# Kernel optimization log

Hardware: AMD Instinct MI355X
Metric: run time of the kernel (lower is better)

Reference implementation:

```python
import jax, jax.numpy as jnp
import numpy as np

B, H, K, NUM_PTR, MAX_LEN = 32768, 896, 2000, 2, 128


def setup_inputs() -> dict:
    key = jax.random.key(0)
    k1, k2, k3 = jax.random.split(key, 3)
    z = jax.random.normal(k1, (B, H), dtype=jnp.float32)
    # codebook init: normal(0, 0.02) as in torch.nn.init.normal_
    emb = 0.02 * jax.random.normal(k2, (K, H), dtype=jnp.float32)
    # pointer heads: two Linear(H, MAX_LEN) layers, stacked
    W = jax.random.normal(k3, (NUM_PTR, MAX_LEN, H), dtype=jnp.float32) / np.float32(np.sqrt(H))
    b = jnp.zeros((NUM_PTR, MAX_LEN), dtype=jnp.float32)
    return {"z": z, "emb": emb, "W": W, "b": b, "prompt_len": 96}


def reference(z, emb, W, b, prompt_len):
    # --- quantize: L2 cdist + argmin + gather + straight-through ---
    # dist[b,k] = ||z_b||^2 - 2 z_b . e_k + ||e_k||^2   -> [B, K]
    dist = (jnp.sum(z * z, axis=1, keepdims=True)
            - 2.0 * (z @ emb.T)
            + jnp.sum(emb * emb, axis=1)[None, :])
    idx = jnp.argmin(dist, axis=1)            # [B]
    z_q = emb[idx]                            # [B, H]
    op_state = z + jax.lax.stop_gradient(z_q - z)
    # --- pointer heads with prompt-length mask ---
    logits = jnp.einsum('bh,plh->bpl', z, W) + b[None, :, :]   # [B, 2, MAX_LEN]
    mask = jnp.where(jnp.arange(logits.shape[-1]) < prompt_len, 0.0, -jnp.inf)
    ptr_logits = logits + mask[None, None, :]
    return op_state, ptr_logits
```

## Files before the change

### kernel.cpp

```cpp
#include <hip/hip_runtime.h>
#include <hip/hip_bf16.h>
#include <cstdint>
#include <cstddef>

#define B_SZ 32768
#define H_SZ 896
#define K_SZ 2000
#define KPAD 2048
#define NPTR_COLS 256
#define NCAT 2304
#define BM 128
#define BN 128
#define BK 32
#define TPS 6

typedef float floatx4 __attribute__((ext_vector_type(4)));
typedef __bf16 bf16x8 __attribute__((ext_vector_type(8)));

#define MASK_NEG 1.0e30f

__device__ inline unsigned short f2bf_rne(float x) {
  unsigned u = __builtin_bit_cast(unsigned, x);
  unsigned r = u + 0x7fffu + ((u >> 16) & 1u);
  return (unsigned short)(r >> 16);
}
__device__ inline float bf2f(unsigned short b) {
  unsigned u = ((unsigned)b) << 16;
  return __builtin_bit_cast(float, u);
}

typedef __attribute__((address_space(1))) void GV;
typedef __attribute__((address_space(3))) void LV;
__device__ inline void load_lds16(const void* gsrc, void* ldst) {
  __builtin_amdgcn_global_load_lds((GV*)gsrc, (LV*)ldst, 16, 0, 0);
}

__global__ __launch_bounds__(256) void convert_kernel(
    const float* __restrict__ emb, const float* __restrict__ W,
    unsigned short* __restrict__ cat_hi, unsigned short* __restrict__ cat_lo,
    float* __restrict__ normE) {
  const int row = blockIdx.x;
  const int tid = threadIdx.x;
  const float* src = nullptr;
  bool zero = false;
  if (row < K_SZ)       src = emb + (size_t)row * H_SZ;
  else if (row < KPAD)  zero = true;
  else                  src = W + (size_t)(row - KPAD) * H_SZ;

  float ss = 0.f;
  for (int c = tid; c < H_SZ; c += 256) {
    float x = zero ? 0.f : src[c];
    unsigned short hb = f2bf_rne(x);
    float hf = bf2f(hb);
    unsigned short lb = f2bf_rne(x - hf);
    cat_hi[(size_t)row * H_SZ + c] = hb;
    cat_lo[(size_t)row * H_SZ + c] = lb;
    ss += x * x;
  }
  #pragma unroll
  for (int off = 32; off > 0; off >>= 1) ss += __shfl_down(ss, off);
  __shared__ float wsum[4];
  const int wave = tid >> 6, lane = tid & 63;
  if (lane == 0) wsum[wave] = ss;
  __syncthreads();
  if (tid == 0 && row < KPAD) normE[row] = wsum[0] + wsum[1] + wsum[2] + wsum[3];
}

__global__ __launch_bounds__(256) void convert_z(
    const float* __restrict__ z,
    unsigned short* __restrict__ zhi, unsigned short* __restrict__ zlo) {
  const size_t t = (size_t)blockIdx.x * 256 + threadIdx.x;
  const float* src = z + t * 8;
  float x[8];
  *(float4*)&x[0] = *(const float4*)src;
  *(float4*)&x[4] = *(const float4*)(src + 4);
  unsigned hv[4], lv[4];
  #pragma unroll
  for (int q = 0; q < 4; ++q) {
    unsigned short h0 = f2bf_rne(x[2 * q]), h1 = f2bf_rne(x[2 * q + 1]);
    float r0 = x[2 * q] - bf2f(h0), r1 = x[2 * q + 1] - bf2f(h1);
    unsigned short l0 = f2bf_rne(r0), l1 = f2bf_rne(r1);
    hv[q] = (unsigned)h0 | ((unsigned)h1 << 16);
    lv[q] = (unsigned)l0 | ((unsigned)l1 << 16);
  }
  *(uint4*)(zhi + t * 8) = make_uint4(hv[0], hv[1], hv[2], hv[3]);
  *(uint4*)(zlo + t * 8) = make_uint4(lv[0], lv[1], lv[2], lv[3]);
}

__global__ __launch_bounds__(256, 2) void main_gemm(
    const unsigned short* __restrict__ zhi,
    const unsigned short* __restrict__ zlo,
    const unsigned short* __restrict__ cat_hi,
    const unsigned short* __restrict__ cat_lo,
    const float* __restrict__ normE,
    const float* __restrict__ bias,
    const int* __restrict__ plen_p,
    float* __restrict__ pmin, int* __restrict__ pidx,
    float* __restrict__ out_logits) {
  __shared__ unsigned short Ahi[BM * BK], Alo[BM * BK];
  __shared__ unsigned short Bhi[BN * BK], Blo[BN * BK];
  __shared__ float red_v[2][BM];
  __shared__ int   red_i[2][BM];

  const int tid = threadIdx.x;
  const int wave = tid >> 6, lane = tid & 63;
  const int wm = wave >> 1, wn = wave & 1;
  const int bx = blockIdx.x, split = blockIdx.y;
  const int b0 = bx * BM;
  const int lrow = lane & 15, lk = lane >> 4;
  const int csw = ((lk ^ ((lrow >> 1) & 3)) << 3);

  const int srow = lane >> 2;
  const int scol = (((lane & 3) ^ ((lane >> 3) & 3)) << 3);

  float minv[16];
  int   mini[16];
  #pragma unroll
  for (int s = 0; s < 16; ++s) { minv[s] = 3.4e38f; mini[s] = 0; }

  const unsigned short* pa_hi[2];
  const unsigned short* pa_lo[2];
  #pragma unroll
  for (int s = 0; s < 2; ++s) {
    const int seg = wave * 2 + s;
    const size_t off = (size_t)(b0 + seg * 16 + srow) * H_SZ + scol;
    pa_hi[s] = zhi + off;
    pa_lo[s] = zlo + off;
  }

  const int t0 = split * TPS;
  for (int tt = t0; tt < t0 + TPS; ++tt) {
    const int n0 = tt * BN;
    const unsigned short* pb_hi[2];
    const unsigned short* pb_lo[2];
    #pragma unroll
    for (int s = 0; s < 2; ++s) {
      const int seg = wave * 2 + s;
      const size_t off = (size_t)(n0 + seg * 16 + srow) * H_SZ + scol;
      pb_hi[s] = cat_hi + off;
      pb_lo[s] = cat_lo + off;
    }

    floatx4 acc[4][4];
    #pragma unroll
    for (int i = 0; i < 4; ++i)
      #pragma unroll
      for (int j = 0; j < 4; ++j) acc[i][j] = (floatx4){0.f, 0.f, 0.f, 0.f};

    for (int kk = 0; kk < H_SZ; kk += BK) {
      #pragma unroll
      for (int s = 0; s < 2; ++s) {
        const int seg = wave * 2 + s;
        load_lds16(pa_hi[s] + kk, &Ahi[seg * 512]);
        load_lds16(pa_lo[s] + kk, &Alo[seg * 512]);
        load_lds16(pb_hi[s] + kk, &Bhi[seg * 512]);
        load_lds16(pb_lo[s] + kk, &Blo[seg * 512]);
      }
      __syncthreads();

      bf16x8 ah[4], al[4], bh[4], bl[4];
      #pragma unroll
      for (int i = 0; i < 4; ++i) {
        const int r = (wm * 64 + i * 16 + lrow) * BK + csw;
        ah[i] = *(const bf16x8*)&Ahi[r];
        al[i] = *(const bf16x8*)&Alo[r];
      }
      #pragma unroll
      for (int j = 0; j < 4; ++j) {
        const int r = (wn * 64 + j * 16 + lrow) * BK + csw;
        bh[j] = *(const bf16x8*)&Bhi[r];
        bl[j] = *(const bf16x8*)&Blo[r];
      }
      #pragma unroll
      for (int i = 0; i < 4; ++i)
        #pragma unroll
        for (int j = 0; j < 4; ++j) {
          acc[i][j] = __builtin_amdgcn_mfma_f32_16x16x32_bf16(ah[i], bh[j], acc[i][j], 0, 0, 0);
          acc[i][j] = __builtin_amdgcn_mfma_f32_16x16x32_bf16(ah[i], bl[j], acc[i][j], 0, 0, 0);
          acc[i][j] = __builtin_amdgcn_mfma_f32_16x16x32_bf16(al[i], bh[j], acc[i][j], 0, 0, 0);
        }
      __syncthreads();
    }

    if (tt < 16) {
      #pragma unroll
      for (int j = 0; j < 4; ++j) {
        const int k = n0 + wn * 64 + j * 16 + lrow;
        const float nE = normE[k];
        const bool valid = (k < K_SZ);
        #pragma unroll
        for (int i = 0; i < 4; ++i)
          #pragma unroll
          for (int r = 0; r < 4; ++r) {
            float v = nE - 2.0f * acc[i][j][r];
            if (!valid) v = 3.4e38f;
            const int s = i * 4 + r;
            if (v < minv[s]) { minv[s] = v; mini[s] = k; }
          }
      }
    } else {
      const int plen = *plen_p;
      #pragma unroll
      for (int j = 0; j < 4; ++j) {
        const int c = (n0 - KPAD) + wn * 64 + j * 16 + lrow;
        const float bv = bias[c];
        const bool masked = ((c & 127) >= plen);
        #pragma unroll
        for (int i = 0; i < 4; ++i) {
          const int growbase = b0 + wm * 64 + i * 16 + lk * 4;
          #pragma unroll
          for (int r = 0; r < 4; ++r) {
            const float val = masked ? -MASK_NEG : (acc[i][j][r] + bv);
            out_logits[(size_t)(growbase + r) * NPTR_COLS + c] = val;
          }
        }
      }
    }
  }

  #pragma unroll
  for (int s = 0; s < 16; ++s) {
    float v = minv[s]; int id = mini[s];
    #pragma unroll
    for (int m = 1; m < 16; m <<= 1) {
      const float ov = __shfl_xor(v, m);
      const int   oid = __shfl_xor(id, m);
      if (ov < v || (ov == v && oid < id)) { v = ov; id = oid; }
    }
    if (lrow == 0) {
      const int row_local = wm * 64 + (s >> 2) * 16 + lk * 4 + (s & 3);
      red_v[wn][row_local] = v;
      red_i[wn][row_local] = id;
    }
  }
  __syncthreads();
  if (tid < BM) {
    const float v0 = red_v[0][tid], v1 = red_v[1][tid];
    float v; int id;
    if (v1 < v0) { v = v1; id = red_i[1][tid]; }
    else         { v = v0; id = red_i[0][tid]; }
    pmin[(size_t)split * B_SZ + b0 + tid] = v;
    pidx[(size_t)split * B_SZ + b0 + tid] = id;
  }
}

__global__ __launch_bounds__(256) void merge_gather(
    const float* __restrict__ z, const float* __restrict__ emb,
    const float* __restrict__ pmin, const int* __restrict__ pidx,
    float* __restrict__ out0) {
  const int row = blockIdx.x;
  float v = pmin[row];
  int  id = pidx[row];
  const float v1 = pmin[B_SZ + row];
  if (v1 < v) { v = v1; id = pidx[B_SZ + row]; }
  const float v2 = pmin[2 * (size_t)B_SZ + row];
  if (v2 < v) { v = v2; id = pidx[2 * (size_t)B_SZ + row]; }
  const float4* e4 = (const float4*)(emb + (size_t)id * H_SZ);
  const float4* z4 = (const float4*)(z + (size_t)row * H_SZ);
  float4* o4 = (float4*)(out0 + (size_t)row * H_SZ);
  const int t = threadIdx.x;
  if (t < H_SZ / 4) {
    const float4 zz = z4[t], ee = e4[t];
    float4 r;
    r.x = zz.x + (ee.x - zz.x);
    r.y = zz.y + (ee.y - zz.y);
    r.z = zz.z + (ee.z - zz.z);
    r.w = zz.w + (ee.w - zz.w);
    o4[t] = r;
  }
}

extern "C" void kernel_launch(void* const* d_in, const int* in_sizes, int n_in,
                              void* d_out, int out_size, void* d_ws, size_t ws_size,
                              hipStream_t stream) {
  const float* z    = (const float*)d_in[0];
  const float* emb  = (const float*)d_in[1];
  const float* W    = (const float*)d_in[2];
  const float* bias = (const float*)d_in[3];
  const int*   plen = (const int*)d_in[4];
  float* out = (float*)d_out;

  char* ws = (char*)d_ws;
  unsigned short* cat_hi = (unsigned short*)(ws);
  unsigned short* cat_lo = (unsigned short*)(ws + 4128768);
  float* normE = (float*)(ws + 8257536);
  float* pmin  = (float*)(ws + 8265728);
  int*   pidx  = (int*)(ws + 8658944);

  unsigned short* zhi = (unsigned short*)out;
  unsigned short* zlo = zhi + (size_t)B_SZ * H_SZ;
  float* out_logits = out + (size_t)B_SZ * H_SZ;

  convert_kernel<<<dim3(NCAT), dim3(256), 0, stream>>>(emb, W, cat_hi, cat_lo, normE);
  convert_z<<<dim3(B_SZ * H_SZ / (256 * 8)), dim3(256), 0, stream>>>(z, zhi, zlo);
  main_gemm<<<dim3(B_SZ / BM, 3), dim3(256), 0, stream>>>(
      zhi, zlo, cat_hi, cat_lo, normE, bias, plen, pmin, pidx, out_logits);
  merge_gather<<<dim3(B_SZ), dim3(256), 0, stream>>>(z, emb, pmin, pidx, out);
}
```

Measured before the change: 744.8 us.

## Use 256x256 tiles with double-buffered LDS pipeline and one N-tile per block

Replaces the 128x128 tile GEMM with 512-thread blocks computing 256x256 tiles. Global-to-LDS loads are double-buffered so the next K-slice is prefetched while the MFMAs run, and s_setprio is used around the MFMA phases. The grid changes from 3 splits that each loop over 6 N-tiles to 9 N-tile blocks per M-tile, so the argmin now merges 8 partials. The two conversion kernels are fused into one launch to save a kernel launch. The larger tiles raise register and LDS pressure, and the per-sub-step barriers add synchronization overhead.

After: 668.5 us. 1.11x faster.

```diff
diff --git a/kernel.cpp b/kernel.cpp
--- a/kernel.cpp
+++ b/kernel.cpp
@@ -9,10 +9,11 @@
 #define KPAD 2048
 #define NPTR_COLS 256
 #define NCAT 2304
-#define BM 128
-#define BN 128
+#define BM 256
+#define BN 256
 #define BK 32
-#define TPS 6
+#define NKS (H_SZ / BK)
+#define NT_ARG 8
 
 typedef float floatx4 __attribute__((ext_vector_type(4)));
 typedef __bf16 bf16x8 __attribute__((ext_vector_type(8)));
@@ -35,59 +36,60 @@
   __builtin_amdgcn_global_load_lds((GV*)gsrc, (LV*)ldst, 16, 0, 0);
 }
 
-__global__ __launch_bounds__(256) void convert_kernel(
+__global__ __launch_bounds__(256) void convert_all(
     const float* __restrict__ emb, const float* __restrict__ W,
+    const float* __restrict__ z,
     unsigned short* __restrict__ cat_hi, unsigned short* __restrict__ cat_lo,
-    float* __restrict__ normE) {
-  const int row = blockIdx.x;
+    float* __restrict__ normE,
+    unsigned short* __restrict__ zhi, unsigned short* __restrict__ zlo) {
+  const int bid = blockIdx.x;
   const int tid = threadIdx.x;
-  const float* src = nullptr;
-  bool zero = false;
-  if (row < K_SZ)       src = emb + (size_t)row * H_SZ;
-  else if (row < KPAD)  zero = true;
-  else                  src = W + (size_t)(row - KPAD) * H_SZ;
-
-  float ss = 0.f;
-  for (int c = tid; c < H_SZ; c += 256) {
-    float x = zero ? 0.f : src[c];
-    unsigned short hb = f2bf_rne(x);
-    float hf = bf2f(hb);
-    unsigned short lb = f2bf_rne(x - hf);
-    cat_hi[(size_t)row * H_SZ + c] = hb;
-    cat_lo[(size_t)row * H_SZ + c] = lb;
-    ss += x * x;
-  }
-  #pragma unroll
-  for (int off = 32; off > 0; off >>= 1) ss += __shfl_down(ss, off);
-  __shared__ float wsum[4];
-  const int wave = tid >> 6, lane = tid & 63;
-  if (lane == 0) wsum[wave] = ss;
-  __syncthreads();
-  if (tid == 0 && row < KPAD) normE[row] = wsum[0] + wsum[1] + wsum[2] + wsum[3];
-}
-
-__global__ __launch_bounds__(256) void convert_z(
-    const float* __restrict__ z,
-    unsigned short* __restrict__ zhi, unsigned short* __restrict__ zlo) {
-  const size_t t = (size_t)blockIdx.x * 256 + threadIdx.x;
-  const float* src = z + t * 8;
-  float x[8];
-  *(float4*)&x[0] = *(const float4*)src;
-  *(float4*)&x[4] = *(const float4*)(src + 4);
-  unsigned hv[4], lv[4];
-  #pragma unroll
-  for (int q = 0; q < 4; ++q) {
-    unsigned short h0 = f2bf_rne(x[2 * q]), h1 = f2bf_rne(x[2 * q + 1]);
-    float r0 = x[2 * q] - bf2f(h0), r1 = x[2 * q + 1] - bf2f(h1);
-    unsigned short l0 = f2bf_rne(r0), l1 = f2bf_rne(r1);
-    hv[q] = (unsigned)h0 | ((unsigned)h1 << 16);
-    lv[q] = (unsigned)l0 | ((unsigned)l1 << 16);
-  }
-  *(uint4*)(zhi + t * 8) = make_uint4(hv[0], hv[1], hv[2], hv[3]);
-  *(uint4*)(zlo + t * 8) = make_uint4(lv[0], lv[1], lv[2], lv[3]);
-}
-
-__global__ __launch_bounds__(256, 2) void main_gemm(
+  if (bid < NCAT) {
+    const int row = bid;
+    const float* src = nullptr;
+    bool zero = false;
+    if (row < K_SZ)       src = emb + (size_t)row * H_SZ;
+    else if (row < KPAD)  zero = true;
+    else                  src = W + (size_t)(row - KPAD) * H_SZ;
+
+    float ss = 0.f;
+    for (int c = tid; c < H_SZ; c += 256) {
+      float x = zero ? 0.f : src[c];
+      unsigned short hb = f2bf_rne(x);
+      float hf = bf2f(hb);
+      unsigned short lb = f2bf_rne(x - hf);
+      cat_hi[(size_t)row * H_SZ + c] = hb;
+      cat_lo[(size_t)row * H_SZ + c] = lb;
+      ss += x * x;
+    }
+    #pragma unroll
+    for (int off = 32; off > 0; off >>= 1) ss += __shfl_down(ss, off);
+    __shared__ float wsum[4];
+    const int wave = tid >> 6, lane = tid & 63;
+    if (lane == 0) wsum[wave] = ss;
+    __syncthreads();
+    if (tid == 0 && row < KPAD) normE[row] = wsum[0] + wsum[1] + wsum[2] + wsum[3];
+  } else {
+    const size_t t = (size_t)(bid - NCAT) * 256 + tid;
+    const float* src = z + t * 8;
+    float x[8];
+    *(float4*)&x[0] = *(const float4*)src;
+    *(float4*)&x[4] = *(const float4*)(src + 4);
+    unsigned hv[4], lv[4];
+    #pragma unroll
+    for (int q = 0; q < 4; ++q) {
+      unsigned short h0 = f2bf_rne(x[2 * q]), h1 = f2bf_rne(x[2 * q + 1]);
+      float r0 = x[2 * q] - bf2f(h0), r1 = x[2 * q + 1] - bf2f(h1);
+      unsigned short l0 = f2bf_rne(r0), l1 = f2bf_rne(r1);
+      hv[q] = (unsigned)h0 | ((unsigned)h1 << 16);
+      lv[q] = (unsigned)l0 | ((unsigned)l1 << 16);
+    }
+    *(uint4*)(zhi + t * 8) = make_uint4(hv[0], hv[1], hv[2], hv[3]);
+    *(uint4*)(zlo + t * 8) = make_uint4(lv[0], lv[1], lv[2], lv[3]);
+  }
+}
+
+__global__ __launch_bounds__(512, 2) void main_gemm(
     const unsigned short* __restrict__ zhi,
     const unsigned short* __restrict__ zlo,
     const unsigned short* __restrict__ cat_hi,
@@ -97,150 +99,211 @@
     const int* __restrict__ plen_p,
     float* __restrict__ pmin, int* __restrict__ pidx,
     float* __restrict__ out_logits) {
-  __shared__ unsigned short Ahi[BM * BK], Alo[BM * BK];
-  __shared__ unsigned short Bhi[BN * BK], Blo[BN * BK];
-  __shared__ float red_v[2][BM];
-  __shared__ int   red_i[2][BM];
+  __shared__ unsigned short ldsA[2][2][BM * BK];
+  __shared__ unsigned short ldsB[2][2][BN * BK];
+  __shared__ float red_v[4][BM];
+  __shared__ int   red_i[4][BM];
 
   const int tid = threadIdx.x;
   const int wave = tid >> 6, lane = tid & 63;
-  const int wm = wave >> 1, wn = wave & 1;
-  const int bx = blockIdx.x, split = blockIdx.y;
-  const int b0 = bx * BM;
+  const int wm = wave >> 2, wn = wave & 3;
+  const int m0 = blockIdx.x * BM;
+  const int nt = blockIdx.y;
+  const int n0 = nt * BN;
   const int lrow = lane & 15, lk = lane >> 4;
   const int csw = ((lk ^ ((lrow >> 1) & 3)) << 3);
 
   const int srow = lane >> 2;
   const int scol = (((lane & 3) ^ ((lane >> 3) & 3)) << 3);
 
-  float minv[16];
-  int   mini[16];
-  #pragma unroll
-  for (int s = 0; s < 16; ++s) { minv[s] = 3.4e38f; mini[s] = 0; }
-
-  const unsigned short* pa_hi[2];
-  const unsigned short* pa_lo[2];
+  size_t offA[2], offB[2];
   #pragma unroll
   for (int s = 0; s < 2; ++s) {
     const int seg = wave * 2 + s;
-    const size_t off = (size_t)(b0 + seg * 16 + srow) * H_SZ + scol;
-    pa_hi[s] = zhi + off;
-    pa_lo[s] = zlo + off;
-  }
-
-  const int t0 = split * TPS;
-  for (int tt = t0; tt < t0 + TPS; ++tt) {
-    const int n0 = tt * BN;
-    const unsigned short* pb_hi[2];
-    const unsigned short* pb_lo[2];
-    #pragma unroll
-    for (int s = 0; s < 2; ++s) {
-      const int seg = wave * 2 + s;
-      const size_t off = (size_t)(n0 + seg * 16 + srow) * H_SZ + scol;
-      pb_hi[s] = cat_hi + off;
-      pb_lo[s] = cat_lo + off;
-    }
-
-    floatx4 acc[4][4];
+    offA[s] = (size_t)(m0 + seg * 16 + srow) * H_SZ + scol;
+    offB[s] = (size_t)(n0 + seg * 16 + srow) * H_SZ + scol;
+  }
+
+  auto STAGE = [&](int b, int s, int kk) {
+    const int seg = wave * 2 + s;
+    load_lds16(zhi    + offA[s] + kk, &ldsA[b][0][seg * 512]);
+    load_lds16(zlo    + offA[s] + kk, &ldsA[b][1][seg * 512]);
+    load_lds16(cat_hi + offB[s] + kk, &ldsB[b][0][seg * 512]);
+    load_lds16(cat_lo + offB[s] + kk, &ldsB[b][1][seg * 512]);
+  };
+
+  floatx4 acc[8][4];
+  #pragma unroll
+  for (int i = 0; i < 8; ++i)
+    #pragma unroll
+    for (int j = 0; j < 4; ++j) acc[i][j] = (floatx4){0.f, 0.f, 0.f, 0.f};
+
+  bf16x8 ah[4], al[4], b0h[2], b0l[2], b1h[2], b1l[2];
+
+  auto RD_A = [&](int b, int mhalf) {
+    #pragma unroll
+    for (int i = 0; i < 4; ++i) {
+      const int r = (wm * 128 + (mhalf * 4 + i) * 16 + lrow) * BK + csw;
+      ah[i] = *(const bf16x8*)&ldsA[b][0][r];
+      al[i] = *(const bf16x8*)&ldsA[b][1][r];
+    }
+  };
+  auto RD_B0 = [&](int b, int nhalf) {
+    #pragma unroll
+    for (int j = 0; j < 2; ++j) {
+      const int r = (wn * 64 + (nhalf * 2 + j) * 16 + lrow) * BK + csw;
+      b0h[j] = *(const bf16x8*)&ldsB[b][0][r];
+      b0l[j] = *(const bf16x8*)&ldsB[b][1][r];
+    }
+  };
+  auto RD_B1 = [&](int b, int nhalf) {
+    #pragma unroll
+    for (int j = 0; j < 2; ++j) {
+      const int r = (wn * 64 + (nhalf * 2 + j) * 16 + lrow) * BK + csw;
+      b1h[j] = *(const bf16x8*)&ldsB[b][0][r];
+      b1l[j] = *(const bf16x8*)&ldsB[b][1][r];
+    }
+  };
+
+  STAGE(0, 0, 0);
+  STAGE(0, 1, 0);
+  asm volatile("s_waitcnt vmcnt(0)" ::: "memory");
+  __builtin_amdgcn_s_barrier();
+
+  for (int ks = 0; ks < NKS; ++ks) {
+    const int cur = ks & 1, nxt = cur ^ 1;
+    const int kk1 = (ks + 1) * BK;
+    const bool pf = (ks + 1 < NKS);
+
+    RD_A(cur, 0);
+    RD_B0(cur, 0);
+    if (pf) STAGE(nxt, 0, kk1);
+    __builtin_amdgcn_s_barrier();
+    __builtin_amdgcn_s_setprio(1);
     #pragma unroll
     for (int i = 0; i < 4; ++i)
       #pragma unroll
-      for (int j = 0; j < 4; ++j) acc[i][j] = (floatx4){0.f, 0.f, 0.f, 0.f};
-
-    for (int kk = 0; kk < H_SZ; kk += BK) {
-      #pragma unroll
-      for (int s = 0; s < 2; ++s) {
-        const int seg = wave * 2 + s;
-        load_lds16(pa_hi[s] + kk, &Ahi[seg * 512]);
-        load_lds16(pa_lo[s] + kk, &Alo[seg * 512]);
-        load_lds16(pb_hi[s] + kk, &Bhi[seg * 512]);
-        load_lds16(pb_lo[s] + kk, &Blo[seg * 512]);
-      }
-      __syncthreads();
-
-      bf16x8 ah[4], al[4], bh[4], bl[4];
-      #pragma unroll
-      for (int i = 0; i < 4; ++i) {
-        const int r = (wm * 64 + i * 16 + lrow) * BK + csw;
-        ah[i] = *(const bf16x8*)&Ahi[r];
-        al[i] = *(const bf16x8*)&Alo[r];
-      }
-      #pragma unroll
-      for (int j = 0; j < 4; ++j) {
-        const int r = (wn * 64 + j * 16 + lrow) * BK + csw;
-        bh[j] = *(const bf16x8*)&Bhi[r];
-        bl[j] = *(const bf16x8*)&Blo[r];
-      }
-      #pragma unroll
-      for (int i = 0; i < 4; ++i)
+      for (int j = 0; j < 2; ++j) {
+        floatx4 c = acc[i][j];
+        c = __builtin_amdgcn_mfma_f32_16x16x32_bf16(ah[i], b0h[j], c, 0, 0, 0);
+        c = __builtin_amdgcn_mfma_f32_16x16x32_bf16(ah[i], b0l[j], c, 0, 0, 0);
+        c = __builtin_amdgcn_mfma_f32_16x16x32_bf16(al[i], b0h[j], c, 0, 0, 0);
+        acc[i][j] = c;
+      }
+    __builtin_amdgcn_s_setprio(0);
+    __builtin_amdgcn_s_barrier();
+
+    RD_B1(cur, 1);
+    if (pf) STAGE(nxt, 1, kk1);
+    __builtin_amdgcn_s_barrier();
+    __builtin_amdgcn_s_setprio(1);
+    #pragma unroll
+    for (int i = 0; i < 4; ++i)
+      #pragma unroll
+      for (int j = 0; j < 2; ++j) {
+        floatx4 c = acc[i][2 + j];
+        c = __builtin_amdgcn_mfma_f32_16x16x32_bf16(ah[i], b1h[j], c, 0, 0, 0);
+        c = __builtin_amdgcn_mfma_f32_16x16x32_bf16(ah[i], b1l[j], c, 0, 0, 0);
+        c = __builtin_amdgcn_mfma_f32_16x16x32_bf16(al[i], b1h[j], c, 0, 0, 0);
+        acc[i][2 + j] = c;
+      }
+    __builtin_amdgcn_s_setprio(0);
+    __builtin_amdgcn_s_barrier();
+
+    RD_A(cur, 1);
+    __builtin_amdgcn_s_barrier();
+    __builtin_amdgcn_s_setprio(1);
+    #pragma unroll
+    for (int i = 0; i < 4; ++i)
+      #pragma unroll
+      for (int j = 0; j < 2; ++j) {
+        floatx4 c = acc[4 + i][2 + j];
+        c = __builtin_amdgcn_mfma_f32_16x16x32_bf16(ah[i], b1h[j], c, 0, 0, 0);
+        c = __builtin_amdgcn_mfma_f32_16x16x32_bf16(ah[i], b1l[j], c, 0, 0, 0);
+        c = __builtin_amdgcn_mfma_f32_16x16x32_bf16(al[i], b1h[j], c, 0, 0, 0);
+        acc[4 + i][2 + j] = c;
+      }
+    __builtin_amdgcn_s_setprio(0);
+    __builtin_amdgcn_s_barrier();
+
+    RD_B0(cur, 0);
+    __builtin_amdgcn_s_barrier();
+    __builtin_amdgcn_s_setprio(1);
+    #pragma unroll
+    for (int i = 0; i < 4; ++i)
+      #pragma unroll
+      for (int j = 0; j < 2; ++j) {
+        floatx4 c = acc[4 + i][j];
+        c = __builtin_amdgcn_mfma_f32_16x16x32_bf16(ah[i], b0h[j], c, 0, 0, 0);
+        c = __builtin_amdgcn_mfma_f32_16x16x32_bf16(ah[i], b0l[j], c, 0, 0, 0);
+        c = __builtin_amdgcn_mfma_f32_16x16x32_bf16(al[i], b0h[j], c, 0, 0, 0);
+        acc[4 + i][j] = c;
+      }
+    __builtin_amdgcn_s_setprio(0);
+    if (pf) { asm volatile("s_waitcnt vmcnt(0)" ::: "memory"); }
+    __builtin_amdgcn_s_barrier();
+    __builtin_amdgcn_sched_barrier(0);
+  }
+
+  if (nt < NT_ARG) {
+    float nE[4]; bool valid[4]; int kcol[4];
+    #pragma unroll
+    for (int nj = 0; nj < 4; ++nj) {
+      kcol[nj] = n0 + wn * 64 + nj * 16 + lrow;
+      valid[nj] = (kcol[nj] < K_SZ);
+      nE[nj] = normE[kcol[nj]];
+    }
+    #pragma unroll
+    for (int mi = 0; mi < 8; ++mi) {
+      #pragma unroll
+      for (int r = 0; r < 4; ++r) {
+        float v = 3.4e38f; int id = kcol[0];
         #pragma unroll
-        for (int j = 0; j < 4; ++j) {
-          acc[i][j] = __builtin_amdgcn_mfma_f32_16x16x32_bf16(ah[i], bh[j], acc[i][j], 0, 0, 0);
-          acc[i][j] = __builtin_amdgcn_mfma_f32_16x16x32_bf16(ah[i], bl[j], acc[i][j], 0, 0, 0);
-          acc[i][j] = __builtin_amdgcn_mfma_f32_16x16x32_bf16(al[i], bh[j], acc[i][j], 0, 0, 0);
+        for (int nj = 0; nj < 4; ++nj) {
+          const float vv = valid[nj] ? (nE[nj] - 2.0f * acc[mi][nj][r]) : 3.4e38f;
+          if (vv < v) { v = vv; id = kcol[nj]; }
         }
-      __syncthreads();
-    }
-
-    if (tt < 16) {
-      #pragma unroll
-      for (int j = 0; j < 4; ++j) {
-        const int k = n0 + wn * 64 + j * 16 + lrow;
-        const float nE = normE[k];
-        const bool valid = (k < K_SZ);
         #pragma unroll
-        for (int i = 0; i < 4; ++i)
-          #pragma unroll
-          for (int r = 0; r < 4; ++r) {
-            float v = nE - 2.0f * acc[i][j][r];
-            if (!valid) v = 3.4e38f;
-            const int s = i * 4 + r;
-            if (v < minv[s]) { minv[s] = v; mini[s] = k; }
-          }
-      }
-    } else {
-      const int plen = *plen_p;
-      #pragma unroll
-      for (int j = 0; j < 4; ++j) {
-        const int c = (n0 - KPAD) + wn * 64 + j * 16 + lrow;
-        const float bv = bias[c];
-        const bool masked = ((c & 127) >= plen);
+        for (int m = 1; m < 16; m <<= 1) {
+          const float ov = __shfl_xor(v, m);
+          const int   oid = __shfl_xor(id, m);
+          if (ov < v || (ov == v && oid < id)) { v = ov; id = oid; }
+        }
+        if (lrow == 0) {
+          const int row_local = wm * 128 + mi * 16 + lk * 4 + r;
+          red_v[wn][row_local] = v;
+          red_i[wn][row_local] = id;
+        }
+      }
+    }
+    __syncthreads();
+    if (tid < BM) {
+      float v = red_v[0][tid]; int id = red_i[0][tid];
+      #pragma unroll
+      for (int w = 1; w < 4; ++w) {
+        const float vw = red_v[w][tid];
+        if (vw < v) { v = vw; id = red_i[w][tid]; }
+      }
+      pmin[(size_t)nt * B_SZ + m0 + tid] = v;
+      pidx[(size_t)nt * B_SZ + m0 + tid] = id;
+    }
+  } else {
+    const int plen = *plen_p;
+    #pragma unroll
+    for (int nj = 0; nj < 4; ++nj) {
+      const int c = wn * 64 + nj * 16 + lrow;
+      const float bv = bias[c];
+      const bool masked = ((c & 127) >= plen);
+      #pragma unroll
+      for (int mi = 0; mi < 8; ++mi) {
+        const int growbase = m0 + wm * 128 + mi * 16 + lk * 4;
         #pragma unroll
-        for (int i = 0; i < 4; ++i) {
-          const int growbase = b0 + wm * 64 + i * 16 + lk * 4;
-          #pragma unroll
-          for (int r = 0; r < 4; ++r) {
-            const float val = masked ? -MASK_NEG : (acc[i][j][r] + bv);
-            out_logits[(size_t)(growbase + r) * NPTR_COLS + c] = val;
-          }
+        for (int r = 0; r < 4; ++r) {
+          const float val = masked ? -MASK_NEG : (acc[mi][nj][r] + bv);
+          out_logits[(size_t)(growbase + r) * NPTR_COLS + c] = val;
         }
       }
     }
-  }
-
-  #pragma unroll
-  for (int s = 0; s < 16; ++s) {
-    float v = minv[s]; int id = mini[s];
-    #pragma unroll
-    for (int m = 1; m < 16; m <<= 1) {
-      const float ov = __shfl_xor(v, m);
-      const int   oid = __shfl_xor(id, m);
-      if (ov < v || (ov == v && oid < id)) { v = ov; id = oid; }
-    }
-    if (lrow == 0) {
-      const int row_local = wm * 64 + (s >> 2) * 16 + lk * 4 + (s & 3);
-      red_v[wn][row_local] = v;
-      red_i[wn][row_local] = id;
-    }
-  }
-  __syncthreads();
-  if (tid < BM) {
-    const float v0 = red_v[0][tid], v1 = red_v[1][tid];
-    float v; int id;
-    if (v1 < v0) { v = v1; id = red_i[1][tid]; }
-    else         { v = v0; id = red_i[0][tid]; }
-    pmin[(size_t)split * B_SZ + b0 + tid] = v;
-    pidx[(size_t)split * B_SZ + b0 + tid] = id;
   }
 }
 
@@ -251,10 +314,11 @@
   const int row = blockIdx.x;
   float v = pmin[row];
   int  id = pidx[row];
-  const float v1 = pmin[B_SZ + row];
-  if (v1 < v) { v = v1; id = pidx[B_SZ + row]; }
-  const float v2 = pmin[2 * (size_t)B_SZ + row];
-  if (v2 < v) { v = v2; id = pidx[2 * (size_t)B_SZ + row]; }
+  #pragma unroll
+  for (int t = 1; t < NT_ARG; ++t) {
+    const float vt = pmin[(size_t)t * B_SZ + row];
+    if (vt < v) { v = vt; id = pidx[(size_t)t * B_SZ + row]; }
+  }
   const float4* e4 = (const float4*)(emb + (size_t)id * H_SZ);
   const float4* z4 = (const float4*)(z + (size_t)row * H_SZ);
   float4* o4 = (float4*)(out0 + (size_t)row * H_SZ);
@@ -285,15 +349,15 @@
   unsigned short* cat_lo = (unsigned short*)(ws + 4128768);
   float* normE = (float*)(ws + 8257536);
   float* pmin  = (float*)(ws + 8265728);
-  int*   pidx  = (int*)(ws + 8658944);
+  int*   pidx  = (int*)(ws + 9314304);
 
   unsigned short* zhi = (unsigned short*)out;
   unsigned short* zlo = zhi + (size_t)B_SZ * H_SZ;
   float* out_logits = out + (size_t)B_SZ * H_SZ;
 
-  convert_kernel<<<dim3(NCAT), dim3(256), 0, stream>>>(emb, W, cat_hi, cat_lo, normE);
-  convert_z<<<dim3(B_SZ * H_SZ / (256 * 8)), dim3(256), 0, stream>>>(z, zhi, zlo);
-  main_gemm<<<dim3(B_SZ / BM, 3), dim3(256), 0, stream>>>(
+  convert_all<<<dim3(NCAT + B_SZ * H_SZ / 2048), dim3(256), 0, stream>>>(
+      emb, W, z, cat_hi, cat_lo, normE, zhi, zlo);
+  main_gemm<<<dim3(B_SZ / BM, 9), dim3(512), 0, stream>>>(
       zhi, zlo, cat_hi, cat_lo, normE, bias, plen, pmin, pidx, out_logits);
   merge_gather<<<dim3(B_SZ), dim3(256), 0, stream>>>(z, emb, pmin, pidx, out);
 }
```
